# Kernel tuning notes

Hardware: AMD Instinct MI355X
Metric: run time of the kernel (lower is better)

## Reference

```python
import jax, jax.numpy as jnp
import numpy as np

D_MODEL = 1024
N_HEADS = 32
HEAD_DIM = D_MODEL // N_HEADS
EPS = 1e-5


def setup_inputs() -> dict:
    key = jax.random.key(0)
    ks = jax.random.split(key, 6)
    B, S = 2, 2048
    scale = 1.0 / np.sqrt(D_MODEL)
    return {
        "x": jax.random.normal(ks[0], (B, S, D_MODEL), dtype=jnp.float32),
        "Wqkv_w": jax.random.normal(ks[1], (3 * D_MODEL, D_MODEL), dtype=jnp.float32) * scale,
        "Wqkv_b": jax.random.normal(ks[2], (3 * D_MODEL,), dtype=jnp.float32) * 0.01,
        "gn_w": jnp.ones((D_MODEL,), dtype=jnp.float32),
        "gn_b": jnp.zeros((D_MODEL,), dtype=jnp.float32),
        "out_w": jax.random.normal(ks[3], (D_MODEL, D_MODEL), dtype=jnp.float32) * scale,
        "out_b": jax.random.normal(ks[4], (D_MODEL,), dtype=jnp.float32) * 0.01,
    }


def reference(x, Wqkv_w, Wqkv_b, gn_w, gn_b, out_w, out_b):
    B, S, Dm = x.shape
    H, Dh = N_HEADS, HEAD_DIM
    # QKV projection
    qkv = x @ Wqkv_w.T + Wqkv_b                      # [B,S,3*Dm]
    qkv = qkv.reshape(B, S, 3, H, Dh)
    q, k, v = qkv[:, :, 0], qkv[:, :, 1], qkv[:, :, 2]  # each [B,S,H,Dh]
    # Linear (softmax-free) attention; dropout p=0 -> identity
    a = jnp.einsum('bthd,bshd->bhts', q, k)          # [B,H,S,S]
    ctx = jnp.einsum('bhts,bshd->bthd', a, v)        # [B,S,H,Dh]
    # GroupNorm(num_groups=H, num_channels=Dm) on transposed (B, Dm, S):
    # normalizes jointly over (Dh channels, S positions) per (batch, group)
    g = ctx.transpose(0, 2, 3, 1)                    # [B,H,Dh,S]
    mean = g.mean(axis=(2, 3), keepdims=True)
    var = ((g - mean) ** 2).mean(axis=(2, 3), keepdims=True)
    gh = (g - mean) * jax.lax.rsqrt(var + EPS)
    gh = gh * gn_w.reshape(H, Dh, 1) + gn_b.reshape(H, Dh, 1)
    ctx = gh.transpose(0, 3, 1, 2).reshape(B, S, Dm)  # back to [B,S,Dm]
    return ctx @ out_w.T + out_b
```

## Files before the change

### kernel.cpp

```cpp
#include <hip/hip_runtime.h>
#include <hip/hip_bf16.h>
#include <stdint.h>

typedef unsigned short ushort_t;
typedef __attribute__((ext_vector_type(4))) float f32x4;
typedef __attribute__((ext_vector_type(8))) short short8;

#define SS 2048
#define ROWS 4096
#define EPS 1e-5f

__device__ __forceinline__ unsigned short f2bf(float f) {
  unsigned int u = __float_as_uint(f);
  u += 0x7FFF + ((u >> 16) & 1);
  return (unsigned short)(u >> 16);
}
__device__ __forceinline__ float bf2f(short s) {
  return __uint_as_float(((unsigned int)(unsigned short)s) << 16);
}

#define GLDS16(g, l)                                                        \
  __builtin_amdgcn_global_load_lds((__attribute__((address_space(1))) void*)(g), \
                                   (__attribute__((address_space(3))) void*)(l), 16, 0, 0)

__global__ __launch_bounds__(256) void f2b2_kernel(const float* __restrict__ a,
                                                   ushort_t* __restrict__ oa, int n4a,
                                                   const float* __restrict__ b,
                                                   ushort_t* __restrict__ ob, int n4b) {
  const int stride = gridDim.x * blockDim.x;
  const int total = n4a + n4b;
  for (int i = blockIdx.x * blockDim.x + threadIdx.x; i < total; i += stride) {
    const float4 v = (i < n4a) ? reinterpret_cast<const float4*>(a)[i]
                               : reinterpret_cast<const float4*>(b)[i - n4a];
    ushort4 o;
    o.x = f2bf(v.x); o.y = f2bf(v.y); o.z = f2bf(v.z); o.w = f2bf(v.w);
    if (i < n4a) reinterpret_cast<ushort4*>(oa)[i] = o;
    else         reinterpret_cast<ushort4*>(ob)[i - n4a] = o;
  }
}

#define MF(d, va, vb) d = __builtin_amdgcn_mfma_f32_16x16x32_bf16(va, vb, d, 0, 0, 0)
#define LD8(p) (*reinterpret_cast<const short8*>(p))

__global__ __launch_bounds__(512, 2) void gemm1_pipe(const ushort_t* __restrict__ A,
                                                     const ushort_t* __restrict__ B,
                                                     const float* __restrict__ bias,
                                                     ushort_t* __restrict__ C) {
  __shared__ __align__(16) ushort_t lds[4 * 14336];
  const int tid = threadIdx.x;
  const int wid = tid >> 6, lane = tid & 63;
  const int bm = blockIdx.x * 256, bn = blockIdx.y * 192;
  const int wm = wid >> 2, wn = wid & 3;

  const int srow = lane >> 2;
  const int scol = ((lane & 3) ^ ((lane >> 3) & 3)) * 8;
  const int widb = (wid < 6) ? wid : 0;
  const ushort_t* gA0 = A + (size_t)(bm + wid * 16 + srow) * 1024 + scol;
  const ushort_t* gA1 = A + (size_t)(bm + (8 + wid) * 16 + srow) * 1024 + scol;
  const ushort_t* gB0 = B + (size_t)(bn + widb * 16 + srow) * 1024 + scol;
  const ushort_t* gB1 = B + (size_t)(bn + (6 + widb) * 16 + srow) * 1024 + scol;

  const int lf = lane & 15, kf = lane >> 4;
  const int flip = ((lane >> 1) & 3) << 4;
  const int aBase = (((wm * 128 + lf) * 64 + kf * 16) ^ flip) >> 1;
  const int bBase = ((((wn * 48 + lf) * 64 + kf * 16) ^ flip) >> 1) + 8192;

  f32x4 acc[8][3] = {};

#define STAGE_A(t)                                                           \
  { ushort_t* d = lds + (((t) & 3) * 14336);                                 \
    GLDS16(gA0 + (t) * 32, d + wid * 512);                                   \
    GLDS16(gA1 + (t) * 32, d + (8 + wid) * 512); }
#define STAGE_B(t)                                                           \
  if (wid < 6) { ushort_t* d = lds + (((t) & 3) * 14336) + 8192;             \
    GLDS16(gB0 + (t) * 32, d + wid * 512);                                   \
    GLDS16(gB1 + (t) * 32, d + (6 + wid) * 512); }

  STAGE_A(0) STAGE_B(0)
  STAGE_A(1) STAGE_B(1)
  STAGE_A(2) STAGE_B(2)
  if (wid < 6) { asm volatile("s_waitcnt vmcnt(8)" ::: "memory"); }
  else         { asm volatile("s_waitcnt vmcnt(4)" ::: "memory"); }
  __builtin_amdgcn_s_barrier();
  __builtin_amdgcn_sched_barrier(0);

#define K_TILE(t, DO_STAGE, VM6, VM2)                                        \
  { const ushort_t* Lb = lds + (((t) & 3) * 14336);                          \
    short8 bv0 = LD8(Lb + bBase);                                            \
    short8 bv1 = LD8(Lb + bBase + 512);                                      \
    short8 bv2 = LD8(Lb + bBase + 1024);                                     \
    short8 a0 = LD8(Lb + aBase);                                             \
    short8 a1 = LD8(Lb + aBase + 512);                                       \
    short8 a2 = LD8(Lb + aBase + 1024);                                      \
    short8 a3 = LD8(Lb + aBase + 1536);                                      \
    if (DO_STAGE) STAGE_A((t) + 3)                                           \
    __builtin_amdgcn_s_setprio(1);                                           \
    MF(acc[0][0], a0, bv0); MF(acc[1][0], a1, bv0);                          \
    MF(acc[0][1], a0, bv1); MF(acc[1][1], a1, bv1);                          \
    MF(acc[0][2], a0, bv2); MF(acc[1][2], a1, bv2);                          \
    MF(acc[2][0], a2, bv0); MF(acc[3][0], a3, bv0);                          \
    MF(acc[2][1], a2, bv1); MF(acc[3][1], a3, bv1);                          \
    MF(acc[2][2], a2, bv2); MF(acc[3][2], a3, bv2);                          \
    __builtin_amdgcn_s_setprio(0);                                           \
    a0 = LD8(Lb + aBase + 2048);                                             \
    a1 = LD8(Lb + aBase + 2560);                                             \
    a2 = LD8(Lb + aBase + 3072);                                             \
    a3 = LD8(Lb + aBase + 3584);                                             \
    if (DO_STAGE) STAGE_B((t) + 3)                                           \
    __builtin_amdgcn_s_setprio(1);                                           \
    MF(acc[4][0], a0, bv0); MF(acc[5][0], a1, bv0);                          \
    MF(acc[4][1], a0, bv1); MF(acc[5][1], a1, bv1);                          \
    MF(acc[4][2], a0, bv2); MF(acc[5][2], a1, bv2);                          \
    MF(acc[6][0], a2, bv0); MF(acc[7][0], a3, bv0);                          \
    MF(acc[6][1], a2, bv1); MF(acc[7][1], a3, bv1);                          \
    MF(acc[6][2], a2, bv2); MF(acc[7][2], a3, bv2);                          \
    __builtin_amdgcn_s_setprio(0);                                           \
    __builtin_amdgcn_sched_barrier(0);                                       \
    if (wid < 6) { asm volatile("s_waitcnt vmcnt(" #VM6 ")" ::: "memory"); } \
    else         { asm volatile("s_waitcnt vmcnt(" #VM2 ")" ::: "memory"); } \
    __builtin_amdgcn_s_barrier();                                            \
    __builtin_amdgcn_sched_barrier(0); }

#pragma unroll 1
  for (int t = 0; t < 29; ++t) K_TILE(t, 1, 8, 4)
  K_TILE(29, 0, 4, 2)
  K_TILE(30, 0, 0, 0)
  K_TILE(31, 0, 0, 0)

  const int crow = bm + wm * 128 + (lane >> 4) * 4;
  const int ccol = bn + wn * 48 + (lane & 15);
#pragma unroll
  for (int m = 0; m < 8; ++m)
#pragma unroll
    for (int n = 0; n < 3; ++n) {
      const int col = ccol + n * 16;
      const float bb = bias[col];
#pragma unroll
      for (int j = 0; j < 4; ++j)
        C[(size_t)(crow + m * 16 + j) * 3072 + col] = f2bf(acc[m][n][j] + bb);
    }
#undef K_TILE
#undef STAGE_A
#undef STAGE_B
}

template <int OUTBF16>
__global__ __launch_bounds__(256) void gemm_bt(const ushort_t* __restrict__ A,
                                               const ushort_t* __restrict__ B,
                                               const float* __restrict__ bias,
                                               void* __restrict__ Cv,
                                               int M, int N, int K, int dualB) {
  __shared__ __align__(16) ushort_t As[128 * 32];
  __shared__ __align__(16) ushort_t Bs[128 * 32];
  const int tid = threadIdx.x;
  const int wave = tid >> 6, lane = tid & 63;
  const int bm = blockIdx.x * 128, bn = blockIdx.y * 128;
  if (dualB && bm >= 2048) { B += (size_t)N * K; bias += N; }
  const int wr = (wave >> 1) * 64, wc = (wave & 1) * 64;

  f32x4 acc[4][4] = {};

  const int srow = lane >> 2;
  const int scol = (lane & 3) * 8;
  const ushort_t* ga0 = A + (size_t)(bm + wave * 16 + srow) * K + scol;
  const ushort_t* ga1 = A + (size_t)(bm + 64 + wave * 16 + srow) * K + scol;
  const ushort_t* gb0 = B + (size_t)(bn + wave * 16 + srow) * K + scol;
  const ushort_t* gb1 = B + (size_t)(bn + 64 + wave * 16 + srow) * K + scol;
  ushort_t* la0 = &As[wave * 512];
  ushort_t* la1 = &As[(wave + 4) * 512];
  ushort_t* lb0 = &Bs[wave * 512];
  ushort_t* lb1 = &Bs[(wave + 4) * 512];

  const int aoff = (wr + (lane & 15)) * 32 + (lane >> 4) * 8;
  const int boff = (wc + (lane & 15)) * 32 + (lane >> 4) * 8;

  for (int k0 = 0; k0 < K; k0 += 32) {
    if (k0) __syncthreads();
    GLDS16(ga0 + k0, la0);
    GLDS16(ga1 + k0, la1);
    GLDS16(gb0 + k0, lb0);
    GLDS16(gb1 + k0, lb1);
    __syncthreads();

    short8 av[4], bv[4];
#pragma unroll
    for (int m = 0; m < 4; ++m)
      av[m] = *reinterpret_cast<const short8*>(&As[aoff + m * 16 * 32]);
#pragma unroll
    for (int n = 0; n < 4; ++n)
      bv[n] = *reinterpret_cast<const short8*>(&Bs[boff + n * 16 * 32]);
#pragma unroll
    for (int m = 0; m < 4; ++m)
#pragma unroll
      for (int n = 0; n < 4; ++n)
        acc[m][n] = __builtin_amdgcn_mfma_f32_16x16x32_bf16(av[m], bv[n], acc[m][n], 0, 0, 0);
  }

  const int crow0 = bm + wr + (lane >> 4) * 4;
  const int ccol0 = bn + wc + (lane & 15);
#pragma unroll
  for (int m = 0; m < 4; ++m)
#pragma unroll
    for (int n = 0; n < 4; ++n) {
      const int col = ccol0 + n * 16;
      const float bb = bias[col];
#pragma unroll
      for (int j = 0; j < 4; ++j) {
        const int row = crow0 + m * 16 + j;
        const float val = acc[m][n][j] + bb;
        if constexpr (OUTBF16) {
          ((ushort_t*)Cv)[(size_t)row * N + col] = f2bf(val);
        } else {
          ((float*)Cv)[(size_t)row * N + col] = val;
        }
      }
    }
}

__global__ __launch_bounds__(256) void kv_partial(const ushort_t* __restrict__ qkvb,
                                                  float* __restrict__ KVp) {
  __shared__ float kt[64 * 32];
  __shared__ float vt[64 * 32];
  const int blk = blockIdx.x;
  const int bh = blk >> 5;
  const int ch = blk & 31;
  const int b = bh >> 5, h = bh & 31;
  const int tid = threadIdx.x;
  const int r = tid >> 2, cg = (tid & 3) * 8;
  const ushort_t* kp = qkvb + (size_t)(b * SS + ch * 64 + r) * 3072 + 1024 + h * 32 + cg;
  const short8 k8 = *(const short8*)kp;
  const short8 v8 = *(const short8*)(kp + 1024);
#pragma unroll
  for (int i = 0; i < 8; ++i) {
    kt[r * 32 + cg + i] = bf2f(k8[i]);
    vt[r * 32 + cg + i] = bf2f(v8[i]);
  }
  __syncthreads();
  const int d = tid & 31, eg = tid >> 5;
  float acc[4] = {0.f, 0.f, 0.f, 0.f};
#pragma unroll 8
  for (int ss = 0; ss < 64; ++ss) {
    const float vv = vt[ss * 32 + d];
#pragma unroll
    for (int i = 0; i < 4; ++i)
      acc[i] += kt[ss * 32 + eg * 4 + i] * vv;
  }
  float* o = KVp + ((size_t)bh * 32 + ch) * 1024 + (eg * 4) * 32 + d;
#pragma unroll
  for (int i = 0; i < 4; ++i) o[i * 32] = acc[i];
}

__global__ __launch_bounds__(256) void kv_reduce(const float* __restrict__ KVp,
                                                 float* __restrict__ KV) {
  const int bh = blockIdx.x;
  const int tid = threadIdx.x;
  const float* base = KVp + (size_t)bh * 32768 + tid * 4;
  float4 s = make_float4(0.f, 0.f, 0.f, 0.f);
  for (int c = 0; c < 32; ++c) {
    const float4 v = *(const float4*)(base + c * 1024);
    s.x += v.x; s.y += v.y; s.z += v.z; s.w += v.w;
  }
  *(float4*)&KV[(size_t)bh * 1024 + tid * 4] = s;
}

__global__ __launch_bounds__(256) void ctx_kernel(const ushort_t* __restrict__ qkvb,
                                                  const float* __restrict__ KV,
                                                  ushort_t* __restrict__ ctxb,
                                                  float2* __restrict__ partials) {
  __shared__ float kvs[1024];
  __shared__ float red[8];
  const int blk = blockIdx.x;
  const int bh = blk >> 3, tt = blk & 7;
  const int b = bh >> 5, h = bh & 31;
  const int tid = threadIdx.x;
  for (int i = tid; i < 1024; i += 256) kvs[i] = KV[(size_t)bh * 1024 + i];
  __syncthreads();
  const int t = tt * 256 + tid;
  const ushort_t* qrow = qkvb + ((size_t)(b * SS + t)) * 3072 + h * 32;
  float q[32];
#pragma unroll
  for (int g = 0; g < 4; ++g) {
    const short8 qv = *(const short8*)(qrow + g * 8);
#pragma unroll
    for (int i = 0; i < 8; ++i) q[g * 8 + i] = bf2f(qv[i]);
  }
  float o[32];
#pragma unroll
  for (int d = 0; d < 32; ++d) o[d] = 0.f;
#pragma unroll
  for (int e = 0; e < 32; ++e) {
    const float qe = q[e];
    const float* kr = &kvs[e * 32];
#pragma unroll
    for (int d = 0; d < 32; ++d) o[d] += qe * kr[d];
  }
  float sum = 0.f, sq = 0.f;
#pragma unroll
  for (int d = 0; d < 32; ++d) { sum += o[d]; sq += o[d] * o[d]; }
  ushort_t* crow = ctxb + ((size_t)(b * SS + t)) * 1024 + h * 32;
#pragma unroll
  for (int g = 0; g < 4; ++g) {
    short8 ov;
#pragma unroll
    for (int i = 0; i < 8; ++i) ov[i] = (short)f2bf(o[g * 8 + i]);
    *(short8*)(crow + g * 8) = ov;
  }
#pragma unroll
  for (int off = 32; off > 0; off >>= 1) {
    sum += __shfl_down(sum, off);
    sq  += __shfl_down(sq, off);
  }
  const int wave = tid >> 6, lane = tid & 63;
  if (lane == 0) { red[wave * 2] = sum; red[wave * 2 + 1] = sq; }
  __syncthreads();
  if (tid == 0) {
    const float s = red[0] + red[2] + red[4] + red[6];
    const float q2 = red[1] + red[3] + red[5] + red[7];
    partials[blk] = make_float2(s, q2);
  }
}

__global__ __launch_bounds__(256) void fold_kernel(const float* __restrict__ W2,
                                                   const float* __restrict__ b2,
                                                   const float* __restrict__ gw,
                                                   const float* __restrict__ gb,
                                                   const float2* __restrict__ partials,
                                                   ushort_t* __restrict__ W2s,
                                                   float* __restrict__ bias2) {
  __shared__ float sS[1024], sT[1024];
  __shared__ float sMean[32], sRstd[32];
  const int b = blockIdx.y;
  const int tid = threadIdx.x;
  if (tid < 32) {
    float s = 0.f, q = 0.f;
    for (int i = 0; i < 8; ++i) {
      const float2 p = partials[(b * 32 + tid) * 8 + i];
      s += p.x; q += p.y;
    }
    const float mean = s * (1.f / 65536.f);
    const float var = q * (1.f / 65536.f) - mean * mean;
    sMean[tid] = mean; sRstd[tid] = rsqrtf(var + EPS);
  }
  __syncthreads();
  {
    const int c0 = tid * 4;
    const float mean = sMean[c0 >> 5], rstd = sRstd[c0 >> 5];
    const float4 w = *(const float4*)&gw[c0];
    const float4 g = *(const float4*)&gb[c0];
    sS[c0]     = rstd * w.x;  sT[c0]     = g.x - mean * rstd * w.x;
    sS[c0 + 1] = rstd * w.y;  sT[c0 + 1] = g.y - mean * rstd * w.y;
    sS[c0 + 2] = rstd * w.z;  sT[c0 + 2] = g.z - mean * rstd * w.z;
    sS[c0 + 3] = rstd * w.w;  sT[c0 + 3] = g.w - mean * rstd * w.w;
  }
  __syncthreads();
  const int row = blockIdx.x * 16 + (tid >> 4);
  const int l16 = tid & 15;
  float part = 0.f;
  for (int k = 0; k < 16; ++k) {
    const int c = k * 64 + l16 * 4;
    const float4 w2v = *(const float4*)&W2[(size_t)row * 1024 + c];
    ushort4 o;
    o.x = f2bf(w2v.x * sS[c]);
    o.y = f2bf(w2v.y * sS[c + 1]);
    o.z = f2bf(w2v.z * sS[c + 2]);
    o.w = f2bf(w2v.w * sS[c + 3]);
    *(ushort4*)&W2s[(size_t)b * 1048576 + (size_t)row * 1024 + c] = o;
    part += w2v.x * sT[c] + w2v.y * sT[c + 1] + w2v.z * sT[c + 2] + w2v.w * sT[c + 3];
  }
#pragma unroll
  for (int off = 8; off > 0; off >>= 1) part += __shfl_down(part, off, 16);
  if (l16 == 0) bias2[b * 1024 + row] = b2[row] + part;
}

extern "C" void kernel_launch(void* const* d_in, const int* in_sizes, int n_in,
                              void* d_out, int out_size, void* d_ws, size_t ws_size,
                              hipStream_t stream) {
  const float* x  = (const float*)d_in[0];
  const float* w1 = (const float*)d_in[1];
  const float* b1 = (const float*)d_in[2];
  const float* gw = (const float*)d_in[3];
  const float* gb = (const float*)d_in[4];
  const float* w2 = (const float*)d_in[5];
  const float* b2 = (const float*)d_in[6];
  float* out = (float*)d_out;

  char* ws = (char*)d_ws;
  ushort_t* Xb    = (ushort_t*)(ws);
  float*    KVp   = (float*)(ws);
  ushort_t* W1b   = (ushort_t*)(ws + 8388608);
  ushort_t* qkvb  = (ushort_t*)(ws + 16777216);
  ushort_t* ctxb  = (ushort_t*)(ws + 41943040);
  ushort_t* W2s   = (ushort_t*)(ws + 50331648);
  float*    bias2 = (float*)(ws + 54525952);
  float*    KV    = (float*)(ws + 54534144);
  float2*   partials = (float2*)(ws + 54796288);

  f2b2_kernel<<<2048, 256, 0, stream>>>(x, Xb, ROWS * 1024 / 4, w1, W1b, 3072 * 1024 / 4);
  gemm1_pipe<<<dim3(16, 16), 512, 0, stream>>>(Xb, W1b, b1, qkvb);
  kv_partial<<<2048, 256, 0, stream>>>(qkvb, KVp);
  kv_reduce<<<64, 256, 0, stream>>>(KVp, KV);
  ctx_kernel<<<512, 256, 0, stream>>>(qkvb, KV, ctxb, partials);
  fold_kernel<<<dim3(64, 2), 256, 0, stream>>>(w2, b2, gw, gb, partials, W2s, bias2);
  gemm_bt<0><<<dim3(32, 8), 256, 0, stream>>>(ctxb, W2s, bias2, out, ROWS, 1024, 1024, 1);
}
```

Baseline: 95.36 us.

## Replace output GEMM with 4-stage pipelined, LDS-swizzled 64x128 tile kernel

Result: faster. 88.92 us (-6.8%).

```diff
diff --git a/kernel.cpp b/kernel.cpp
--- a/kernel.cpp
+++ b/kernel.cpp
@@ -144,77 +144,81 @@
 #undef STAGE_B
 }
 
-template <int OUTBF16>
-__global__ __launch_bounds__(256) void gemm_bt(const ushort_t* __restrict__ A,
-                                               const ushort_t* __restrict__ B,
-                                               const float* __restrict__ bias,
-                                               void* __restrict__ Cv,
-                                               int M, int N, int K, int dualB) {
-  __shared__ __align__(16) ushort_t As[128 * 32];
-  __shared__ __align__(16) ushort_t Bs[128 * 32];
-  const int tid = threadIdx.x;
-  const int wave = tid >> 6, lane = tid & 63;
-  const int bm = blockIdx.x * 128, bn = blockIdx.y * 128;
-  if (dualB && bm >= 2048) { B += (size_t)N * K; bias += N; }
-  const int wr = (wave >> 1) * 64, wc = (wave & 1) * 64;
-
-  f32x4 acc[4][4] = {};
+__global__ __launch_bounds__(256, 2) void gemm2_pipe(const ushort_t* __restrict__ A,
+                                                     const ushort_t* __restrict__ B,
+                                                     const float* __restrict__ bias,
+                                                     float* __restrict__ C) {
+  __shared__ __align__(16) ushort_t lds[4 * 6144];
+  const int tid = threadIdx.x;
+  const int wid = tid >> 6, lane = tid & 63;
+  const int bm = blockIdx.x * 64, bn = blockIdx.y * 128;
+  if (bm >= 2048) { B += (size_t)1024 * 1024; bias += 1024; }
+  const int wm = wid >> 1, wn = wid & 1;
 
   const int srow = lane >> 2;
-  const int scol = (lane & 3) * 8;
-  const ushort_t* ga0 = A + (size_t)(bm + wave * 16 + srow) * K + scol;
-  const ushort_t* ga1 = A + (size_t)(bm + 64 + wave * 16 + srow) * K + scol;
-  const ushort_t* gb0 = B + (size_t)(bn + wave * 16 + srow) * K + scol;
-  const ushort_t* gb1 = B + (size_t)(bn + 64 + wave * 16 + srow) * K + scol;
-  ushort_t* la0 = &As[wave * 512];
-  ushort_t* la1 = &As[(wave + 4) * 512];
-  ushort_t* lb0 = &Bs[wave * 512];
-  ushort_t* lb1 = &Bs[(wave + 4) * 512];
-
-  const int aoff = (wr + (lane & 15)) * 32 + (lane >> 4) * 8;
-  const int boff = (wc + (lane & 15)) * 32 + (lane >> 4) * 8;
-
-  for (int k0 = 0; k0 < K; k0 += 32) {
-    if (k0) __syncthreads();
-    GLDS16(ga0 + k0, la0);
-    GLDS16(ga1 + k0, la1);
-    GLDS16(gb0 + k0, lb0);
-    GLDS16(gb1 + k0, lb1);
-    __syncthreads();
-
-    short8 av[4], bv[4];
-#pragma unroll
-    for (int m = 0; m < 4; ++m)
-      av[m] = *reinterpret_cast<const short8*>(&As[aoff + m * 16 * 32]);
-#pragma unroll
-    for (int n = 0; n < 4; ++n)
-      bv[n] = *reinterpret_cast<const short8*>(&Bs[boff + n * 16 * 32]);
-#pragma unroll
-    for (int m = 0; m < 4; ++m)
-#pragma unroll
-      for (int n = 0; n < 4; ++n)
-        acc[m][n] = __builtin_amdgcn_mfma_f32_16x16x32_bf16(av[m], bv[n], acc[m][n], 0, 0, 0);
-  }
-
-  const int crow0 = bm + wr + (lane >> 4) * 4;
-  const int ccol0 = bn + wc + (lane & 15);
-#pragma unroll
-  for (int m = 0; m < 4; ++m)
+  const int scol = ((lane & 3) ^ ((lane >> 3) & 3)) * 8;
+  const ushort_t* gA  = A + (size_t)(bm + wid * 16 + srow) * 1024 + scol;
+  const ushort_t* gB0 = B + (size_t)(bn + wid * 16 + srow) * 1024 + scol;
+  const ushort_t* gB1 = B + (size_t)(bn + (4 + wid) * 16 + srow) * 1024 + scol;
+
+  const int lf = lane & 15, kf = lane >> 4;
+  const int flip = ((lane >> 1) & 3) << 4;
+  const int aBase = (((wm * 32 + lf) * 64 + kf * 16) ^ flip) >> 1;
+  const int bBase = ((((wn * 64 + lf) * 64 + kf * 16) ^ flip) >> 1) + 2048;
+
+  f32x4 acc[2][4] = {};
+
+#define STAGE2(t)                                                            \
+  { ushort_t* d = lds + (((t) & 3) * 6144);                                  \
+    GLDS16(gA + (t) * 32, d + wid * 512);                                    \
+    GLDS16(gB0 + (t) * 32, d + 2048 + wid * 512);                            \
+    GLDS16(gB1 + (t) * 32, d + 2048 + (4 + wid) * 512); }
+
+  STAGE2(0) STAGE2(1) STAGE2(2)
+  asm volatile("s_waitcnt vmcnt(6)" ::: "memory");
+  __builtin_amdgcn_s_barrier();
+  __builtin_amdgcn_sched_barrier(0);
+
+#define K_TILE2(t, DO_STAGE, VM)                                             \
+  { const ushort_t* Lb = lds + (((t) & 3) * 6144);                           \
+    short8 bv0 = LD8(Lb + bBase);                                            \
+    short8 bv1 = LD8(Lb + bBase + 512);                                      \
+    short8 bv2 = LD8(Lb + bBase + 1024);                                     \
+    short8 bv3 = LD8(Lb + bBase + 1536);                                     \
+    short8 a0 = LD8(Lb + aBase);                                             \
+    short8 a1 = LD8(Lb + aBase + 512);                                       \
+    if (DO_STAGE) STAGE2((t) + 3)                                            \
+    __builtin_amdgcn_s_setprio(1);                                           \
+    MF(acc[0][0], a0, bv0); MF(acc[1][0], a1, bv0);                          \
+    MF(acc[0][1], a0, bv1); MF(acc[1][1], a1, bv1);                          \
+    MF(acc[0][2], a0, bv2); MF(acc[1][2], a1, bv2);                          \
+    MF(acc[0][3], a0, bv3); MF(acc[1][3], a1, bv3);                          \
+    __builtin_amdgcn_s_setprio(0);                                           \
+    __builtin_amdgcn_sched_barrier(0);                                       \
+    asm volatile("s_waitcnt vmcnt(" #VM ")" ::: "memory");                   \
+    __builtin_amdgcn_s_barrier();                                            \
+    __builtin_amdgcn_sched_barrier(0); }
+
+#pragma unroll 1
+  for (int t = 0; t < 29; ++t) K_TILE2(t, 1, 6)
+  K_TILE2(29, 0, 3)
+  K_TILE2(30, 0, 0)
+  K_TILE2(31, 0, 0)
+
+  const int crow = bm + wm * 32 + (lane >> 4) * 4;
+  const int ccol = bn + wn * 64 + lf;
+#pragma unroll
+  for (int m = 0; m < 2; ++m)
 #pragma unroll
     for (int n = 0; n < 4; ++n) {
-      const int col = ccol0 + n * 16;
+      const int col = ccol + n * 16;
       const float bb = bias[col];
 #pragma unroll
-      for (int j = 0; j < 4; ++j) {
-        const int row = crow0 + m * 16 + j;
-        const float val = acc[m][n][j] + bb;
-        if constexpr (OUTBF16) {
-          ((ushort_t*)Cv)[(size_t)row * N + col] = f2bf(val);
-        } else {
-          ((float*)Cv)[(size_t)row * N + col] = val;
-        }
-      }
+      for (int j = 0; j < 4; ++j)
+        C[(size_t)(crow + m * 16 + j) * 1024 + col] = acc[m][n][j] + bb;
     }
+#undef K_TILE2
+#undef STAGE2
 }
 
 __global__ __launch_bounds__(256) void kv_partial(const ushort_t* __restrict__ qkvb,
@@ -401,5 +405,5 @@
   kv_reduce<<<64, 256, 0, stream>>>(KVp, KV);
   ctx_kernel<<<512, 256, 0, stream>>>(qkvb, KV, ctxb, partials);
   fold_kernel<<<dim3(64, 2), 256, 0, stream>>>(w2, b2, gw, gb, partials, W2s, bias2);
-  gemm_bt<0><<<dim3(32, 8), 256, 0, stream>>>(ctxb, W2s, bias2, out, ROWS, 1024, 1024, 1);
-}
+  gemm2_pipe<<<dim3(64, 8), 256, 0, stream>>>(ctxb, W2s, bias2, out);
+}
```
